# Kernel optimization log

Measured on AMD Instinct MI355X. Metric: run time of the kernel, lower is better.

Reference implementation:

```python
import jax, jax.numpy as jnp
import numpy as np

N = 100000
E = 1600000
D_IN = 128
F = 128


def _glorot(key, shape, scale=1.0):
    fan_in, fan_out = shape
    std = jnp.sqrt(2.0 / (fan_in + fan_out))
    return jax.random.normal(key, shape, dtype=jnp.float32) * std * scale


def setup_inputs() -> dict:
    key = jax.random.key(0)
    ks = jax.random.split(key, 10)
    h = jax.random.normal(ks[0], (N, D_IN), dtype=jnp.float32)
    # ensure every node appears as a row (src) so degree >= 1 (no inf in deg**-0.5)
    src_extra = jax.random.randint(ks[1], (E - N,), 0, N, dtype=jnp.int32)
    edge_src = jnp.concatenate([jnp.arange(N, dtype=jnp.int32), src_extra])
    edge_dst = jax.random.randint(ks[2], (E,), 0, N, dtype=jnp.int32)
    # faithful to original: fake indices sampled in [0, E) (jnp indexing clamps)
    src_fake = jax.random.randint(ks[3], (E,), 0, E, dtype=jnp.int32)
    dst_fake = jax.random.randint(ks[4], (E,), 0, E, dtype=jnp.int32)
    w_gcn0 = _glorot(ks[5], (D_IN, F))
    w_gcn1 = _glorot(ks[6], (F, F))
    # small scale on rate0 head to keep exp(sum over F dims) finite in fp32
    w_rate0 = _glorot(ks[7], (F, F), scale=0.05)
    w_rate1 = _glorot(ks[8], (F, 1))
    w_alpha = _glorot(ks[9], (F, 1))
    return {"h": h, "w_gcn0": w_gcn0, "w_gcn1": w_gcn1, "w_rate0": w_rate0,
            "w_rate1": w_rate1, "w_alpha": w_alpha, "edge_src": edge_src,
            "edge_dst": edge_dst, "src_fake": src_fake, "dst_fake": dst_fake}


def _gcn(h, W, norm, edge_src, edge_dst):
    h = h * norm                     # [N, d] degree pre-norm
    h = h @ W                        # dense projection
    h = jax.ops.segment_sum(h[edge_dst], edge_src, num_segments=N)  # a @ h
    return h * norm                  # degree post-norm


def reference(h, w_gcn0, w_gcn1, w_rate0, w_rate1, w_alpha,
              edge_src, edge_dst, src_fake, dst_fake):
    ones = jnp.ones((E,), dtype=h.dtype)
    deg = jax.ops.segment_sum(ones, edge_src, num_segments=N)  # row sums of a
    norm = (deg ** -0.5)[:, None]

    h = _gcn(h, w_gcn0, norm, edge_src, edge_dst)
    h = _gcn(h, w_gcn1, norm, edge_src, edge_dst)

    rate0 = h @ w_rate0   # [N, F]
    rate1 = h @ w_rate1   # [N, 1]
    alpha = h @ w_alpha   # [N, 1]

    src, dst = edge_src, edge_dst
    rate0_real = jnp.exp((rate0[src] + rate0[dst]).sum(-1))
    rate1_real = jnp.exp((rate1[src] + rate1[dst]).sum(-1))
    alpha_real = jax.nn.sigmoid((alpha[src] * alpha[dst]).sum(-1) / alpha.shape[-1] ** 0.5)

    # faithful to original (including rate0+rate1 mix and /shape (not sqrt) in alpha_fake)
    rate0_fake = jnp.exp((rate0[src_fake] + rate1[dst_fake]).sum(-1))
    rate1_fake = jnp.exp((rate1[src_fake] + rate1[dst_fake]).sum(-1))
    alpha_fake = jax.nn.sigmoid((alpha[src] * alpha[dst_fake]).sum(-1) / alpha.shape[-1])

    return jnp.stack([rate0_real, rate1_real, alpha_real,
                      rate0_fake, rate1_fake, alpha_fake])  # [6, E]
```

## Files before the change

### kernel.cpp

```cpp
#include <hip/hip_runtime.h>
#include <hip/hip_bf16.h>
#include <math.h>

#define NN 100000
#define EE 1600000
#define KB 256
#define RR 391
#define CAP 8192


__global__ __launch_bounds__(256) void k_initcur(int* __restrict__ gcur) {
    gcur[threadIdx.x] = threadIdx.x * CAP;
}


__global__ __launch_bounds__(256) void k_partA(const int* __restrict__ src, const int* __restrict__ dst,
                                               int* __restrict__ gcur, unsigned int* __restrict__ pk, int E) {
    __shared__ int cnt[KB];
    __shared__ int base[KB];
    int t = threadIdx.x;
    int e0 = blockIdx.x * 4096;
    cnt[t] = 0;
    __syncthreads();
    unsigned int pkv[16];
    int bkt[16];
    #pragma unroll
    for (int i = 0; i < 16; ++i) {
        int e = e0 + i * 256 + t;
        if (e < E) {
            int s = src[e];
            int d = dst[e];
            int b = s / RR;
            bkt[i] = b;
            pkv[i] = (unsigned int)d | ((unsigned int)(s - b * RR) << 17);
            atomicAdd(&cnt[b], 1);
        } else {
            bkt[i] = -1;
        }
    }
    __syncthreads();
    base[t] = (cnt[t] > 0) ? atomicAdd(&gcur[t], cnt[t]) : 0;
    __syncthreads();
    cnt[t] = 0;
    __syncthreads();
    #pragma unroll
    for (int i = 0; i < 16; ++i) {
        if (bkt[i] >= 0) {
            int r = atomicAdd(&cnt[bkt[i]], 1);
            int pos = base[bkt[i]] + r;
            if (pos < (bkt[i] + 1) * CAP) pk[pos] = pkv[i];
        }
    }
}


__global__ __launch_bounds__(128) void k_pmat(const float* __restrict__ w_gcn0,
                                              const float* __restrict__ w_gcn1,
                                              const float* __restrict__ w_rate0,
                                              const float* __restrict__ w_rate1,
                                              const float* __restrict__ w_alpha,
                                              float* __restrict__ Pt0, float* __restrict__ Pt1,
                                              float* __restrict__ Pt2) {
    __shared__ float V0[128], V1[128], V2[128];
    __shared__ float Q0[128], Q1[128], Q2[128];
    int t = threadIdx.x;
    float s = 0.f;
    for (int j = 0; j < 128; ++j) s += w_rate0[t * 128 + j];
    V0[t] = s;
    V1[t] = w_rate1[t];
    V2[t] = w_alpha[t];
    __syncthreads();
    {
        float q0 = 0.f, q1 = 0.f, q2 = 0.f;
        for (int k = 0; k < 128; ++k) {
            float w = w_gcn1[t * 128 + k];
            q0 += w * V0[k];
            q1 += w * V1[k];
            q2 += w * V2[k];
        }
        Q0[t] = q0; Q1[t] = q1; Q2[t] = q2;
    }
    __syncthreads();
    {
        float p0 = 0.f, p1 = 0.f, p2 = 0.f;
        for (int m = 0; m < 128; ++m) {
            float w = w_gcn0[t * 128 + m];
            p0 += w * Q0[m];
            p1 += w * Q1[m];
            p2 += w * Q2[m];
        }
        Pt0[t] = p0; Pt1[t] = p1; Pt2[t] = p2;
    }
}


__global__ __launch_bounds__(1024) void k_cnt_proj(const unsigned int* __restrict__ pk,
                                                   const int* __restrict__ gcur,
                                                   const float* __restrict__ h,
                                                   const float* __restrict__ Pt0, const float* __restrict__ Pt1,
                                                   const float* __restrict__ Pt2,
                                                   float* __restrict__ nrm, float4* __restrict__ w4, int n) {
    __shared__ int c[RR];
    __shared__ float s_nrm[RR];
    __shared__ float sP0[128], sP1[128], sP2[128];
    int b = blockIdx.x;
    int t = threadIdx.x;
    int nlo = b * RR;
    int nhi = nlo + RR; if (nhi > n) nhi = n;
    if (nlo >= n) return;
    int nn = nhi - nlo;
    if (t < 128) { sP0[t] = Pt0[t]; sP1[t] = Pt1[t]; sP2[t] = Pt2[t]; }
    for (int i = t; i < RR; i += 1024) c[i] = 0;
    __syncthreads();
    int P0 = b * CAP;
    int m = gcur[b] - P0;
    for (int i = t; i < m; i += 1024) atomicAdd(&c[pk[P0 + i] >> 17], 1);
    __syncthreads();
    for (int i = t; i < nn; i += 1024) {
        float nv = rsqrtf((float)c[i]);
        s_nrm[i] = nv;
        nrm[nlo + i] = nv;
    }
    __syncthreads();
    int hw = t >> 5;
    int l32 = t & 31;
    int c4 = l32 * 4;
    float4 c0 = *(const float4*)(sP0 + c4);
    float4 c1 = *(const float4*)(sP1 + c4);
    float4 c2 = *(const float4*)(sP2 + c4);
    for (int i0 = 0; i0 < nn; i0 += 32) {
        int i = i0 + hw;
        if (i >= nn) break;
        int node = nlo + i;
        float4 hv = *(const float4*)(h + (size_t)node * 128 + c4);
        float p0 = hv.x * c0.x + hv.y * c0.y + hv.z * c0.z + hv.w * c0.w;
        float p1 = hv.x * c1.x + hv.y * c1.y + hv.z * c1.z + hv.w * c1.w;
        float p2 = hv.x * c2.x + hv.y * c2.y + hv.z * c2.z + hv.w * c2.w;
        #pragma unroll
        for (int off = 16; off > 0; off >>= 1) {
            p0 += __shfl_down(p0, off, 32);
            p1 += __shfl_down(p1, off, 32);
            p2 += __shfl_down(p2, off, 32);
        }
        if (l32 == 0) {
            float nv = s_nrm[i];
            w4[node] = make_float4(nv * p0, nv * p1, nv * p2, 0.f);
        }
    }
}


__global__ __launch_bounds__(1024) void k_agg(const unsigned int* __restrict__ pk,
                                              const int* __restrict__ gcur,
                                              const float4* __restrict__ T, const float* __restrict__ nrm,
                                              float4* __restrict__ outv, int n, int mode) {
    __shared__ float s0[RR], s1[RR], s2[RR];
    int b = blockIdx.x;
    int t = threadIdx.x;
    int nlo = b * RR;
    int nhi = nlo + RR; if (nhi > n) nhi = n;
    if (nlo >= n) return;
    for (int i = t; i < RR; i += 1024) { s0[i] = 0.f; s1[i] = 0.f; s2[i] = 0.f; }
    __syncthreads();
    int P0 = b * CAP;
    int m = gcur[b] - P0;
    for (int i = t; i < m; i += 1024) {
        unsigned int w = pk[P0 + i];
        int srel = (int)(w >> 17);
        float4 v = T[w & 0x1FFFFu];
        atomicAdd(&s0[srel], v.x);
        atomicAdd(&s1[srel], v.y);
        atomicAdd(&s2[srel], v.z);
    }
    __syncthreads();
    int nn = nhi - nlo;
    for (int i = t; i < nn; i += 1024) {
        int node = nlo + i;
        float nv = nrm[node];
        float sc = (mode == 1) ? nv * nv : nv;
        outv[node] = make_float4(sc * s0[i], sc * s1[i], sc * s2[i], 0.f);
    }
}


__global__ __launch_bounds__(256) void k_edge_out(const int* __restrict__ esrc, const int* __restrict__ edst,
                                                  const int* __restrict__ sfake, const int* __restrict__ dfake,
                                                  const float4* __restrict__ p4, float* __restrict__ out,
                                                  int E, int n) {
    int e = blockIdx.x * 256 + threadIdx.x;
    if (e >= E) return;
    int s = esrc[e], d = edst[e];
    int sf = sfake[e]; sf = sf < 0 ? 0 : (sf >= n ? n - 1 : sf);
    int df = dfake[e]; df = df < 0 ? 0 : (df >= n ? n - 1 : df);
    float4 ps = p4[s], pd = p4[d], psf = p4[sf], pdf = p4[df];
    out[e]                 = expf(ps.x + pd.x);
    out[(size_t)E + e]     = expf(ps.y + pd.y);
    out[(size_t)2 * E + e] = 1.f / (1.f + expf(-(ps.z * pd.z)));
    out[(size_t)3 * E + e] = expf(psf.x + 128.f * pdf.y);
    out[(size_t)4 * E + e] = expf(psf.y + pdf.y);
    out[(size_t)5 * E + e] = 1.f / (1.f + expf(-(ps.z * pdf.z)));
}


extern "C" void kernel_launch(void* const* d_in, const int* in_sizes, int n_in,
                              void* d_out, int out_size, void* d_ws, size_t ws_size,
                              hipStream_t stream) {
    const float* h       = (const float*)d_in[0];
    const float* w_gcn0  = (const float*)d_in[1];
    const float* w_gcn1  = (const float*)d_in[2];
    const float* w_rate0 = (const float*)d_in[3];
    const float* w_rate1 = (const float*)d_in[4];
    const float* w_alpha = (const float*)d_in[5];
    const int* edge_src  = (const int*)d_in[6];
    const int* edge_dst  = (const int*)d_in[7];
    const int* src_fake  = (const int*)d_in[8];
    const int* dst_fake  = (const int*)d_in[9];
    float* out = (float*)d_out;

    const int N = NN, E = EE;

    char* p = (char*)d_ws;
    auto alloc = [&](size_t bytes) {
        char* r = p;
        p += (bytes + 255) & ~(size_t)255;
        return r;
    };
    unsigned int* pk = (unsigned int*)alloc((size_t)KB * CAP * 4);
    int* gcur   = (int*)alloc(KB * 4);
    float* nrm  = (float*)alloc((size_t)N * 4);
    float4* w4  = (float4*)alloc((size_t)N * 16);
    float4* z4  = (float4*)alloc((size_t)N * 16);
    float4* p4  = (float4*)alloc((size_t)N * 16);
    float* Pt0  = (float*)alloc(512);
    float* Pt1  = (float*)alloc(512);
    float* Pt2  = (float*)alloc(512);

    int ebl4k = (E + 4095) / 4096;
    int ebl = (E + 255) / 256;

    k_initcur<<<1, KB, 0, stream>>>(gcur);
    k_partA<<<ebl4k, 256, 0, stream>>>(edge_src, edge_dst, gcur, pk, E);
    k_pmat<<<1, 128, 0, stream>>>(w_gcn0, w_gcn1, w_rate0, w_rate1, w_alpha, Pt0, Pt1, Pt2);
    k_cnt_proj<<<KB, 1024, 0, stream>>>(pk, gcur, h, Pt0, Pt1, Pt2, nrm, w4, N);
    k_agg<<<KB, 1024, 0, stream>>>(pk, gcur, w4, nrm, z4, N, 1);
    k_agg<<<KB, 1024, 0, stream>>>(pk, gcur, z4, nrm, p4, N, 2);
    k_edge_out<<<ebl, 256, 0, stream>>>(edge_src, edge_dst, src_fake, dst_fake, p4, out, E, N);
}
```

Baseline: 241.6 us.

## Vectorize edge loads/stores, merge small kernels, batch aggregation loads

Replaces the cursor-init kernel with a memset and folds the weight-product computation into block 0 of the partition kernel, cutting launches. The partition kernel now reads edges as int4 and records each edge's rank during the count pass, dropping the second atomic pass. The aggregation kernel issues up to 8 independent packed and gathered loads per thread before doing the shared atomics, to raise memory-level parallelism. The edge-output kernel handles 4 edges per thread with int4 index loads and float4 stores. The aggregation assumes at most 8 slices of 1024 per bucket (CAP), and the int4 loads assume E is divisible by 4.

New measurement: 249.4 us. 3.2% more time.

```diff
diff --git a/kernel.cpp b/kernel.cpp
--- a/kernel.cpp
+++ b/kernel.cpp
@@ -9,87 +9,80 @@
 #define CAP 8192
 
 
-__global__ __launch_bounds__(256) void k_initcur(int* __restrict__ gcur) {
-    gcur[threadIdx.x] = threadIdx.x * CAP;
-}
-
-
 __global__ __launch_bounds__(256) void k_partA(const int* __restrict__ src, const int* __restrict__ dst,
-                                               int* __restrict__ gcur, unsigned int* __restrict__ pk, int E) {
+                                               int* __restrict__ gcur, unsigned int* __restrict__ pk, int E,
+                                               const float* __restrict__ w_gcn0, const float* __restrict__ w_gcn1,
+                                               const float* __restrict__ w_rate0, const float* __restrict__ w_rate1,
+                                               const float* __restrict__ w_alpha, float* __restrict__ P) {
     __shared__ int cnt[KB];
     __shared__ int base[KB];
     int t = threadIdx.x;
     int e0 = blockIdx.x * 4096;
+    int rem = E - e0;
     cnt[t] = 0;
     __syncthreads();
     unsigned int pkv[16];
     int bkt[16];
-    #pragma unroll
-    for (int i = 0; i < 16; ++i) {
-        int e = e0 + i * 256 + t;
-        if (e < E) {
-            int s = src[e];
-            int d = dst[e];
-            int b = s / RR;
-            bkt[i] = b;
-            pkv[i] = (unsigned int)d | ((unsigned int)(s - b * RR) << 17);
-            atomicAdd(&cnt[b], 1);
+    int rnk[16];
+    const int4* src4 = (const int4*)(src + e0);
+    const int4* dst4 = (const int4*)(dst + e0);
+    #pragma unroll
+    for (int j = 0; j < 4; ++j) {
+        int o = t * 16 + j * 4;
+        if (o < rem) {
+            int4 s4 = src4[t * 4 + j];
+            int4 d4 = dst4[t * 4 + j];
+            int ss[4] = {s4.x, s4.y, s4.z, s4.w};
+            int dd[4] = {d4.x, d4.y, d4.z, d4.w};
+            #pragma unroll
+            for (int k = 0; k < 4; ++k) {
+                int b = ss[k] / RR;
+                int idx = j * 4 + k;
+                bkt[idx] = b;
+                pkv[idx] = (unsigned int)dd[k] | ((unsigned int)(ss[k] - b * RR) << 17);
+                rnk[idx] = atomicAdd(&cnt[b], 1);
+            }
         } else {
-            bkt[i] = -1;
+            #pragma unroll
+            for (int k = 0; k < 4; ++k) bkt[j * 4 + k] = -1;
         }
     }
     __syncthreads();
     base[t] = (cnt[t] > 0) ? atomicAdd(&gcur[t], cnt[t]) : 0;
-    __syncthreads();
-    cnt[t] = 0;
     __syncthreads();
     #pragma unroll
     for (int i = 0; i < 16; ++i) {
         if (bkt[i] >= 0) {
-            int r = atomicAdd(&cnt[bkt[i]], 1);
-            int pos = base[bkt[i]] + r;
-            if (pos < (bkt[i] + 1) * CAP) pk[pos] = pkv[i];
-        }
-    }
-}
-
-
-__global__ __launch_bounds__(128) void k_pmat(const float* __restrict__ w_gcn0,
-                                              const float* __restrict__ w_gcn1,
-                                              const float* __restrict__ w_rate0,
-                                              const float* __restrict__ w_rate1,
-                                              const float* __restrict__ w_alpha,
-                                              float* __restrict__ Pt0, float* __restrict__ Pt1,
-                                              float* __restrict__ Pt2) {
-    __shared__ float V0[128], V1[128], V2[128];
-    __shared__ float Q0[128], Q1[128], Q2[128];
-    int t = threadIdx.x;
-    float s = 0.f;
-    for (int j = 0; j < 128; ++j) s += w_rate0[t * 128 + j];
-    V0[t] = s;
-    V1[t] = w_rate1[t];
-    V2[t] = w_alpha[t];
-    __syncthreads();
-    {
-        float q0 = 0.f, q1 = 0.f, q2 = 0.f;
-        for (int k = 0; k < 128; ++k) {
-            float w = w_gcn1[t * 128 + k];
-            q0 += w * V0[k];
-            q1 += w * V1[k];
-            q2 += w * V2[k];
-        }
-        Q0[t] = q0; Q1[t] = q1; Q2[t] = q2;
-    }
-    __syncthreads();
-    {
-        float p0 = 0.f, p1 = 0.f, p2 = 0.f;
-        for (int m = 0; m < 128; ++m) {
-            float w = w_gcn0[t * 128 + m];
-            p0 += w * Q0[m];
-            p1 += w * Q1[m];
-            p2 += w * Q2[m];
-        }
-        Pt0[t] = p0; Pt1[t] = p1; Pt2[t] = p2;
+            int rel = base[bkt[i]] + rnk[i];
+            if (rel < CAP) pk[bkt[i] * CAP + rel] = pkv[i];
+        }
+    }
+    if (blockIdx.x == 0) {
+        __shared__ float V0[128], V1[128], V2[128];
+        __shared__ float Q0[128], Q1[128], Q2[128];
+        if (t < 128) {
+            float s = 0.f;
+            for (int j = 0; j < 128; ++j) s += w_rate0[t * 128 + j];
+            V0[t] = s; V1[t] = w_rate1[t]; V2[t] = w_alpha[t];
+        }
+        __syncthreads();
+        if (t < 128) {
+            float q0 = 0.f, q1 = 0.f, q2 = 0.f;
+            for (int k = 0; k < 128; ++k) {
+                float w = w_gcn1[t * 128 + k];
+                q0 += w * V0[k]; q1 += w * V1[k]; q2 += w * V2[k];
+            }
+            Q0[t] = q0; Q1[t] = q1; Q2[t] = q2;
+        }
+        __syncthreads();
+        if (t < 128) {
+            float p0 = 0.f, p1 = 0.f, p2 = 0.f;
+            for (int m = 0; m < 128; ++m) {
+                float w = w_gcn0[t * 128 + m];
+                p0 += w * Q0[m]; p1 += w * Q1[m]; p2 += w * Q2[m];
+            }
+            P[t] = p0; P[128 + t] = p1; P[256 + t] = p2;
+        }
     }
 }
 
@@ -97,23 +90,22 @@
 __global__ __launch_bounds__(1024) void k_cnt_proj(const unsigned int* __restrict__ pk,
                                                    const int* __restrict__ gcur,
                                                    const float* __restrict__ h,
-                                                   const float* __restrict__ Pt0, const float* __restrict__ Pt1,
-                                                   const float* __restrict__ Pt2,
+                                                   const float* __restrict__ P,
                                                    float* __restrict__ nrm, float4* __restrict__ w4, int n) {
     __shared__ int c[RR];
     __shared__ float s_nrm[RR];
-    __shared__ float sP0[128], sP1[128], sP2[128];
+    __shared__ float sP[384];
     int b = blockIdx.x;
     int t = threadIdx.x;
     int nlo = b * RR;
     int nhi = nlo + RR; if (nhi > n) nhi = n;
     if (nlo >= n) return;
     int nn = nhi - nlo;
-    if (t < 128) { sP0[t] = Pt0[t]; sP1[t] = Pt1[t]; sP2[t] = Pt2[t]; }
+    if (t < 384) sP[t] = P[t];
     for (int i = t; i < RR; i += 1024) c[i] = 0;
     __syncthreads();
     int P0 = b * CAP;
-    int m = gcur[b] - P0;
+    int m = gcur[b]; if (m > CAP) m = CAP;
     for (int i = t; i < m; i += 1024) atomicAdd(&c[pk[P0 + i] >> 17], 1);
     __syncthreads();
     for (int i = t; i < nn; i += 1024) {
@@ -125,9 +117,9 @@
     int hw = t >> 5;
     int l32 = t & 31;
     int c4 = l32 * 4;
-    float4 c0 = *(const float4*)(sP0 + c4);
-    float4 c1 = *(const float4*)(sP1 + c4);
-    float4 c2 = *(const float4*)(sP2 + c4);
+    float4 c0 = *(const float4*)(sP + c4);
+    float4 c1 = *(const float4*)(sP + 128 + c4);
+    float4 c2 = *(const float4*)(sP + 256 + c4);
     for (int i0 = 0; i0 < nn; i0 += 32) {
         int i = i0 + hw;
         if (i >= nn) break;
@@ -163,14 +155,28 @@
     for (int i = t; i < RR; i += 1024) { s0[i] = 0.f; s1[i] = 0.f; s2[i] = 0.f; }
     __syncthreads();
     int P0 = b * CAP;
-    int m = gcur[b] - P0;
-    for (int i = t; i < m; i += 1024) {
-        unsigned int w = pk[P0 + i];
-        int srel = (int)(w >> 17);
-        float4 v = T[w & 0x1FFFFu];
-        atomicAdd(&s0[srel], v.x);
-        atomicAdd(&s1[srel], v.y);
-        atomicAdd(&s2[srel], v.z);
+    int m = gcur[b]; if (m > CAP) m = CAP;
+    unsigned int w[8];
+    float4 v[8];
+    bool ok[8];
+    #pragma unroll
+    for (int j = 0; j < 8; ++j) {
+        int i = t + j * 1024;
+        ok[j] = i < m;
+        if (ok[j]) w[j] = pk[P0 + i];
+    }
+    #pragma unroll
+    for (int j = 0; j < 8; ++j) {
+        if (ok[j]) v[j] = T[w[j] & 0x1FFFFu];
+    }
+    #pragma unroll
+    for (int j = 0; j < 8; ++j) {
+        if (ok[j]) {
+            int srel = (int)(w[j] >> 17);
+            atomicAdd(&s0[srel], v[j].x);
+            atomicAdd(&s1[srel], v[j].y);
+            atomicAdd(&s2[srel], v[j].z);
+        }
     }
     __syncthreads();
     int nn = nhi - nlo;
@@ -187,18 +193,37 @@
                                                   const int* __restrict__ sfake, const int* __restrict__ dfake,
                                                   const float4* __restrict__ p4, float* __restrict__ out,
                                                   int E, int n) {
-    int e = blockIdx.x * 256 + threadIdx.x;
+    int e = (blockIdx.x * 256 + threadIdx.x) * 4;
     if (e >= E) return;
-    int s = esrc[e], d = edst[e];
-    int sf = sfake[e]; sf = sf < 0 ? 0 : (sf >= n ? n - 1 : sf);
-    int df = dfake[e]; df = df < 0 ? 0 : (df >= n ? n - 1 : df);
-    float4 ps = p4[s], pd = p4[d], psf = p4[sf], pdf = p4[df];
-    out[e]                 = expf(ps.x + pd.x);
-    out[(size_t)E + e]     = expf(ps.y + pd.y);
-    out[(size_t)2 * E + e] = 1.f / (1.f + expf(-(ps.z * pd.z)));
-    out[(size_t)3 * E + e] = expf(psf.x + 128.f * pdf.y);
-    out[(size_t)4 * E + e] = expf(psf.y + pdf.y);
-    out[(size_t)5 * E + e] = 1.f / (1.f + expf(-(ps.z * pdf.z)));
+    int4 s4 = *(const int4*)(esrc + e);
+    int4 d4 = *(const int4*)(edst + e);
+    int4 sf4 = *(const int4*)(sfake + e);
+    int4 df4 = *(const int4*)(dfake + e);
+    int ss[4] = {s4.x, s4.y, s4.z, s4.w};
+    int dd[4] = {d4.x, d4.y, d4.z, d4.w};
+    int sf[4] = {sf4.x, sf4.y, sf4.z, sf4.w};
+    int df[4] = {df4.x, df4.y, df4.z, df4.w};
+    float4 o0, o1, o2, o3, o4o, o5;
+    float* po0 = (float*)&o0; float* po1 = (float*)&o1; float* po2 = (float*)&o2;
+    float* po3 = (float*)&o3; float* po4 = (float*)&o4o; float* po5 = (float*)&o5;
+    #pragma unroll
+    for (int k = 0; k < 4; ++k) {
+        int sfc = sf[k] < 0 ? 0 : (sf[k] >= n ? n - 1 : sf[k]);
+        int dfc = df[k] < 0 ? 0 : (df[k] >= n ? n - 1 : df[k]);
+        float4 ps = p4[ss[k]], pd = p4[dd[k]], psf = p4[sfc], pdf = p4[dfc];
+        po0[k] = expf(ps.x + pd.x);
+        po1[k] = expf(ps.y + pd.y);
+        po2[k] = 1.f / (1.f + expf(-(ps.z * pd.z)));
+        po3[k] = expf(psf.x + 128.f * pdf.y);
+        po4[k] = expf(psf.y + pdf.y);
+        po5[k] = 1.f / (1.f + expf(-(ps.z * pdf.z)));
+    }
+    *(float4*)(out + e)                 = o0;
+    *(float4*)(out + (size_t)E + e)     = o1;
+    *(float4*)(out + (size_t)2 * E + e) = o2;
+    *(float4*)(out + (size_t)3 * E + e) = o3;
+    *(float4*)(out + (size_t)4 * E + e) = o4o;
+    *(float4*)(out + (size_t)5 * E + e) = o5;
 }
 
 
@@ -231,18 +256,16 @@
     float4* w4  = (float4*)alloc((size_t)N * 16);
     float4* z4  = (float4*)alloc((size_t)N * 16);
     float4* p4  = (float4*)alloc((size_t)N * 16);
-    float* Pt0  = (float*)alloc(512);
-    float* Pt1  = (float*)alloc(512);
-    float* Pt2  = (float*)alloc(512);
+    float* P    = (float*)alloc(384 * 4);
+
+    hipMemsetAsync(gcur, 0, KB * 4, stream);
 
     int ebl4k = (E + 4095) / 4096;
-    int ebl = (E + 255) / 256;
-
-    k_initcur<<<1, KB, 0, stream>>>(gcur);
-    k_partA<<<ebl4k, 256, 0, stream>>>(edge_src, edge_dst, gcur, pk, E);
-    k_pmat<<<1, 128, 0, stream>>>(w_gcn0, w_gcn1, w_rate0, w_rate1, w_alpha, Pt0, Pt1, Pt2);
-    k_cnt_proj<<<KB, 1024, 0, stream>>>(pk, gcur, h, Pt0, Pt1, Pt2, nrm, w4, N);
+
+    k_partA<<<ebl4k, 256, 0, stream>>>(edge_src, edge_dst, gcur, pk, E,
+                                       w_gcn0, w_gcn1, w_rate0, w_rate1, w_alpha, P);
+    k_cnt_proj<<<KB, 1024, 0, stream>>>(pk, gcur, h, P, nrm, w4, N);
     k_agg<<<KB, 1024, 0, stream>>>(pk, gcur, w4, nrm, z4, N, 1);
     k_agg<<<KB, 1024, 0, stream>>>(pk, gcur, z4, nrm, p4, N, 2);
-    k_edge_out<<<ebl, 256, 0, stream>>>(edge_src, edge_dst, src_fake, dst_fake, p4, out, E, N);
-}
+    k_edge_out<<<(E / 4 + 255) / 256, 256, 0, stream>>>(edge_src, edge_dst, src_fake, dst_fake, p4, out, E, N);
+}
```
